# Optimization experiments

Measured on AMD Instinct MI355X. Metric: run time of the kernel, lower is better.

Reference implementation:

```python
import jax, jax.numpy as jnp
import numpy as np

N_MOTIF_PER_CLASS = 8
N_CLASS = 16
N_MOTIF = N_MOTIF_PER_CLASS * N_CLASS
TEMPERATURE = 0.2
TAU = 0.99
K2 = 32
EPS = 1e-4


def setup_inputs() -> dict:
    key = jax.random.key(0)
    k1, k2, k3 = jax.random.split(key, 3)
    N, H = 32768, 1024
    z = jax.random.normal(k1, (N, H), dtype=jnp.float32)
    Motif_Vector = jax.random.normal(k2, (N_MOTIF, H), dtype=jnp.float32)
    y = jax.random.randint(k3, (N,), 0, N_CLASS, dtype=jnp.int64)
    return {"z": z, "Motif_Vector": Motif_Vector, "y": y}


def euclidean_1(X, M):
    # squared euclidean distance via GEMM, then log-ratio similarity
    xp = X @ M.T                                     # [N, n_motif]
    distance = (-2.0 * xp
                + jnp.sum(X * X, axis=1, keepdims=True)
                + jnp.sum(M * M, axis=1)[None, :])
    similarity = jnp.log((distance + 1.0) / (distance + EPS))
    return similarity, distance


def reference(z, Motif_Vector, y):
    similarity, distance = euclidean_1(z, Motif_Vector)

    # mapping: motif j belongs to class j // n_motif_per_class
    motif_class = jnp.arange(N_MOTIF) // N_MOTIF_PER_CLASS   # [n_motif]
    true_motifs = (y[:, None] == motif_class[None, :])       # [N, n_motif]

    # contrastive loss (exact torch math: exp(sim/T), max over positives,
    # sum over negatives)
    sims = jnp.exp(similarity / TEMPERATURE)
    sim_pos = jnp.max(jnp.where(true_motifs, sims, -jnp.inf), axis=1)
    sim_neg_sum = jnp.sum(jnp.where(true_motifs, 0.0, sims), axis=1)
    loss = -jnp.mean(jnp.log(sim_pos / (sim_neg_sum + sim_pos)))

    # update_motif (update_type='topk', weighted_mean=False):
    # torch passes `distance` into filter_similar_graph and argsorts
    # descending, i.e. selects the K2 LARGEST distances among same-class
    # samples (faithful to source).
    masked = jnp.where(true_motifs.T, distance.T, -jnp.inf)  # [n_motif, N]
    _, idx = jax.lax.top_k(masked, K2)                       # [n_motif, K2]
    selected = z[idx]                                        # [n_motif, K2, H]
    new_motif = jnp.mean(selected, axis=1)                   # weights = 1/K2
    new_M = TAU * Motif_Vector + (1.0 - TAU) * new_motif

    return loss, new_M
```

## Files before the change

kernel.cpp:

```cpp
#include <hip/hip_runtime.h>
#include <cstdint>
#include <cmath>

#define NROWS 32768
#define HD    1024
#define NMOT  128
#define NCLS  16
#define KSEL  32
#define EPSV  1e-4f

typedef __attribute__((ext_vector_type(4))) float  f32x4;
typedef __attribute__((ext_vector_type(8))) __bf16 bf16x8;
typedef __attribute__((ext_vector_type(4))) __bf16 bf16x4;
typedef unsigned long long u64;

#define WS_MN   64
#define WS_MVBF 256
#define WS_CD   65792
#define WS_S1K  327936

static __device__ __forceinline__ float dot4(float4 v) {
    return v.x * v.x + v.y * v.y + v.z * v.z + v.w * v.w;
}

static __device__ __forceinline__ bf16x4 cvt4(float4 v) {
    bf16x4 t;
    t[0] = (__bf16)v.x; t[1] = (__bf16)v.y; t[2] = (__bf16)v.z; t[3] = (__bf16)v.w;
    return t;
}

static __device__ __forceinline__ u64 pack_key(float v, int idx) {
    unsigned int b = __float_as_uint(v);
    unsigned int mo = (b & 0x80000000u) ? ~b : (b | 0x80000000u);
    unsigned int khi = ~mo;
    return ((u64)khi << 32) | (unsigned int)idx;
}

__global__ __launch_bounds__(256) void prep_k(const float* __restrict__ mv,
                                              float* __restrict__ wsf,
                                              __bf16* __restrict__ mvbf) {
    const int j = blockIdx.x;
    const int k = threadIdx.x * 4;
    float4 v = *(const float4*)&mv[(size_t)j * HD + k];
    *(bf16x4*)&mvbf[(size_t)j * HD + k] = cvt4(v);
    float s = dot4(v);
#pragma unroll
    for (int o = 1; o < 64; o <<= 1) s += __shfl_xor(s, o, 64);
    __shared__ float red[4];
    if ((threadIdx.x & 63) == 0) red[threadIdx.x >> 6] = s;
    __syncthreads();
    if (threadIdx.x == 0) {
        wsf[WS_MN + j] = red[0] + red[1] + red[2] + red[3];
        if (j == 0) wsf[0] = 0.f;
    }
}

#define BM 64
#define BN 128
#define BK 32
#define NS (HD / BK)
#define SA 40

__global__ __launch_bounds__(256, 2) void gemm_fused(
    const float* __restrict__ z, const __bf16* __restrict__ mvbf,
    const float* __restrict__ mn, float* __restrict__ cd,
    const int* __restrict__ y, float* __restrict__ lossAcc) {
    __shared__ __bf16 As[2][BM * SA];
    __shared__ __bf16 Bs[2][BN * SA];
    __shared__ float  szn[BM];
    __shared__ int    ly[BM];
    __shared__ float  spm[2][BM];
    __shared__ float  sns[2][BM];

    const int tid  = threadIdx.x;
    const int row0 = blockIdx.x * BM;
    const int lane = tid & 63;
    const int wave = tid >> 6;
    const int wr   = wave >> 1;
    const int wc   = wave & 1;
    const int l15  = lane & 15;
    const int quad = lane >> 4;

    const int sq = tid & 7;
    const int sr = tid >> 3;
    const int bq = tid & 3;
    const int br = tid >> 2;

    if (tid < BM) ly[tid] = y[row0 + tid];

    f32x4 acc[2][4];
#pragma unroll
    for (int i = 0; i < 2; ++i)
#pragma unroll
        for (int j = 0; j < 4; ++j) acc[i][j] = (f32x4){0.f, 0.f, 0.f, 0.f};

    float zsq0 = 0.f, zsq1 = 0.f;

    const float*  zb = z + (size_t)(row0 + sr) * HD + sq * 4;
    const __bf16* bb = mvbf + (size_t)br * HD + bq * 8;

    float4 ra0[4], ra1[4];
    bf16x8 rb0[4], rb1[4];
#pragma unroll
    for (int s = 0; s < 4; ++s) {
        ra0[s] = *(const float4*)(zb + s * BK);
        ra1[s] = *(const float4*)(zb + s * BK + 32 * HD);
        rb0[s] = *(const bf16x8*)(bb + s * BK);
        rb1[s] = *(const bf16x8*)(bb + s * BK + 64 * HD);
    }
    *(bf16x4*)&As[0][sr * SA + sq * 4]        = cvt4(ra0[0]);
    *(bf16x4*)&As[0][(sr + 32) * SA + sq * 4] = cvt4(ra1[0]);
    *(bf16x8*)&Bs[0][br * SA + bq * 8]        = rb0[0];
    *(bf16x8*)&Bs[0][(br + 64) * SA + bq * 8] = rb1[0];
    zsq0 += dot4(ra0[0]); zsq1 += dot4(ra1[0]);
    ra0[0] = *(const float4*)(zb + 4 * BK);
    ra1[0] = *(const float4*)(zb + 4 * BK + 32 * HD);
    rb0[0] = *(const bf16x8*)(bb + 4 * BK);
    rb1[0] = *(const bf16x8*)(bb + 4 * BK + 64 * HD);
    __syncthreads();

    for (int it = 0; it < NS / 4; ++it) {
#pragma unroll
        for (int u = 0; u < 4; ++u) {
            const int kt = it * 4 + u;
            const int rbuf = kt & 1;
            const int ko = quad * 8;
            bf16x8 af[2], bfr[4];
#pragma unroll
            for (int i = 0; i < 2; ++i)
                af[i] = *(const bf16x8*)&As[rbuf][(wr * 32 + i * 16 + l15) * SA + ko];
#pragma unroll
            for (int j = 0; j < 4; ++j)
                bfr[j] = *(const bf16x8*)&Bs[rbuf][(wc * 64 + j * 16 + l15) * SA + ko];
            if (kt + 1 < NS) {
                const int w = (kt + 1) & 1;
                const int s = (kt + 1) & 3;
                *(bf16x4*)&As[w][sr * SA + sq * 4]        = cvt4(ra0[s]);
                *(bf16x4*)&As[w][(sr + 32) * SA + sq * 4] = cvt4(ra1[s]);
                *(bf16x8*)&Bs[w][br * SA + bq * 8]        = rb0[s];
                *(bf16x8*)&Bs[w][(br + 64) * SA + bq * 8] = rb1[s];
                zsq0 += dot4(ra0[s]); zsq1 += dot4(ra1[s]);
                if (kt + 5 < NS) {
                    const float*  zn = zb + (kt + 5) * BK;
                    const __bf16* bn = bb + (kt + 5) * BK;
                    ra0[s] = *(const float4*)(zn);
                    ra1[s] = *(const float4*)(zn + 32 * HD);
                    rb0[s] = *(const bf16x8*)(bn);
                    rb1[s] = *(const bf16x8*)(bn + 64 * HD);
                }
            }
#pragma unroll
            for (int i = 0; i < 2; ++i)
#pragma unroll
                for (int j = 0; j < 4; ++j)
                    acc[i][j] = __builtin_amdgcn_mfma_f32_16x16x32_bf16(
                        af[i], bfr[j], acc[i][j], 0, 0, 0);
            __syncthreads();
        }
    }

#pragma unroll
    for (int o = 1; o < 8; o <<= 1) {
        zsq0 += __shfl_xor(zsq0, o, 64);
        zsq1 += __shfl_xor(zsq1, o, 64);
    }
    if (sq == 0) { szn[sr] = zsq0; szn[sr + 32] = zsq1; }
    __syncthreads();

    f32x4 znv[2];
    int rcls[2][4];
#pragma unroll
    for (int i = 0; i < 2; ++i) {
        znv[i] = *(const f32x4*)&szn[wr * 32 + i * 16 + quad * 4];
#pragma unroll
        for (int reg = 0; reg < 4; ++reg)
            rcls[i][reg] = ly[wr * 32 + i * 16 + quad * 4 + reg];
    }
    float pm[2][4], ns[2][4];
#pragma unroll
    for (int i = 0; i < 2; ++i)
#pragma unroll
        for (int reg = 0; reg < 4; ++reg) { pm[i][reg] = 0.f; ns[i][reg] = 0.f; }

#pragma unroll
    for (int j = 0; j < 4; ++j) {
        const int c = wc * 64 + j * 16 + l15;
        const float mc = mn[c];
        const int ccls = c >> 3;
#pragma unroll
        for (int i = 0; i < 2; ++i) {
#pragma unroll
            for (int reg = 0; reg < 4; ++reg) {
                const int row = wr * 32 + i * 16 + quad * 4 + reg;
                float d = znv[i][reg] + mc - 2.f * acc[i][j][reg];
                float r = (d + 1.0f) * __builtin_amdgcn_rcpf(d + EPSV);
                float r2 = r * r;
                float s = r2 * r2 * r;
                if (ccls == rcls[i][reg]) {
                    pm[i][reg] = fmaxf(pm[i][reg], s);
                    cd[(size_t)(row0 + row) * 8 + (c & 7)] = d;
                } else {
                    ns[i][reg] += s;
                }
            }
        }
    }
#pragma unroll
    for (int o = 1; o < 16; o <<= 1) {
#pragma unroll
        for (int i = 0; i < 2; ++i)
#pragma unroll
            for (int reg = 0; reg < 4; ++reg) {
                pm[i][reg] = fmaxf(pm[i][reg], __shfl_xor(pm[i][reg], o, 64));
                ns[i][reg] += __shfl_xor(ns[i][reg], o, 64);
            }
    }
    if (l15 == 0) {
#pragma unroll
        for (int i = 0; i < 2; ++i)
#pragma unroll
            for (int reg = 0; reg < 4; ++reg) {
                const int row = wr * 32 + i * 16 + quad * 4 + reg;
                spm[wc][row] = pm[i][reg];
                sns[wc][row] = ns[i][reg];
            }
    }
    __syncthreads();
    if (tid < BM) {
        float p = fmaxf(spm[0][tid], spm[1][tid]);
        float nsum = sns[0][tid] + sns[1][tid];
        float li = logf((nsum + p) / p);
#pragma unroll
        for (int o = 1; o < 64; o <<= 1) li += __shfl_xor(li, o, 64);
        if (tid == 0) atomicAdd(lossAcc, li);
    }
}

__global__ __launch_bounds__(256) void sel1_k(const int* __restrict__ y,
                                              const float* __restrict__ cd,
                                              u64* __restrict__ s1k) {
    __shared__ u64 keys[512];
    __shared__ int cnt;

    const int bid = blockIdx.x;
    const int j = bid >> 3, chunk = bid & 7;
    const int cls = j >> 3, m8 = j & 7;
    const int tid = threadIdx.x;
    const int lane = tid & 63;
    if (tid == 0) cnt = 0;
    __syncthreads();

    const int base = chunk * 4096;
#pragma unroll
    for (int t = 0; t < 16; ++t) {
        const int i = base + t * 256 + tid;
        const bool pred = (y[i] == cls);
        const u64 m = __ballot(pred);
        int wbase = 0;
        if (lane == 0 && m) wbase = atomicAdd(&cnt, (int)__popcll(m));
        wbase = __shfl(wbase, 0, 64);
        if (pred) {
            const int p = wbase + (int)__popcll(m & ((1ull << lane) - 1ull));
            if (p < 512) keys[p] = pack_key(cd[(size_t)i * 8 + m8], i);
        }
    }
    __syncthreads();
    const int n = cnt < 512 ? cnt : 512;
    for (int t = tid; t < 512; t += 256)
        if (t >= n) keys[t] = ~0ull;
    __syncthreads();

    for (int k = 2; k <= 512; k <<= 1) {
        for (int jj = k >> 1; jj > 0; jj >>= 1) {
            const int i  = ((tid & ~(jj - 1)) << 1) | (tid & (jj - 1));
            const int ix = i | jj;
            const u64 A = keys[i], B = keys[ix];
            const bool up = ((i & k) == 0);
            if ((A > B) == up) { keys[i] = B; keys[ix] = A; }
            __syncthreads();
        }
    }
    if (tid < KSEL) s1k[(size_t)bid * KSEL + tid] = keys[tid];
}

__global__ __launch_bounds__(256) void merge_k(
    const float* __restrict__ z, const float* __restrict__ mv,
    const u64* __restrict__ s1k, const float* __restrict__ lossAcc,
    float* __restrict__ out) {
    __shared__ u64 keys[256];
    __shared__ int sel[KSEL];

    const int b = blockIdx.x;
    const int j = b >> 2, q = b & 3;
    const int tid = threadIdx.x;
    keys[tid] = s1k[(size_t)j * 256 + tid];
    __syncthreads();

    for (int k = 2; k <= 256; k <<= 1) {
        for (int jj = k >> 1; jj > 0; jj >>= 1) {
            if (tid < 128) {
                const int i  = ((tid & ~(jj - 1)) << 1) | (tid & (jj - 1));
                const int ix = i | jj;
                const u64 A = keys[i], B = keys[ix];
                const bool up = ((i & k) == 0);
                if ((A > B) == up) { keys[i] = B; keys[ix] = A; }
            }
            __syncthreads();
        }
    }
    if (tid < KSEL) sel[tid] = (int)(keys[tid] & 0xFFFFFFFFu);
    __syncthreads();

    const int h = q * 256 + tid;
    float s = 0.f;
#pragma unroll 8
    for (int r = 0; r < KSEL; ++r) s += z[(size_t)sel[r] * HD + h];
    out[1 + (size_t)j * HD + h] =
        0.99f * mv[(size_t)j * HD + h] + 0.01f * (s * (1.0f / KSEL));
    if (b == 0 && tid == 0) out[0] = lossAcc[0] * (1.0f / NROWS);
}

extern "C" void kernel_launch(void* const* d_in, const int* in_sizes, int n_in,
                              void* d_out, int out_size, void* d_ws, size_t ws_size,
                              hipStream_t stream) {
    const float* z  = (const float*)d_in[0];
    const float* mv = (const float*)d_in[1];
    const int*   y  = (const int*)d_in[2];
    float* out = (float*)d_out;
    float* wsf = (float*)d_ws;
    float*  mn   = wsf + WS_MN;
    __bf16* mvbf = (__bf16*)(wsf + WS_MVBF);
    float*  cd   = wsf + WS_CD;
    u64*    s1k  = (u64*)(wsf + WS_S1K);

    hipLaunchKernelGGL(prep_k,     dim3(NMOT),       dim3(256), 0, stream, mv, wsf, mvbf);
    hipLaunchKernelGGL(gemm_fused, dim3(NROWS / BM), dim3(256), 0, stream, z, mvbf, mn, cd, y, wsf);
    hipLaunchKernelGGL(sel1_k,     dim3(NMOT * 8),   dim3(256), 0, stream, y, cd, s1k);
    hipLaunchKernelGGL(merge_k,    dim3(NMOT * 4),   dim3(256), 0, stream, z, mv, s1k, wsf, out);
}
```

Measured before the change: 236.7 us.

## Precompute per-class row index lists and restructure two-stage top-k selection

Builds per-class, per-chunk lists of row indices once in the prep kernel, with 256 extra blocks scanning y. The first selection stage then gathers distances from the list instead of each of 128 motifs rescanning y, and sorts only 256 keys per block across 16 chunks. The merge stage sorts 512 candidates instead of 256. This cuts redundant scans of y and shrinks the first-stage sort, at the cost of a larger merge sort and an assumption that each chunk holds at most 256 same-class rows.

```diff
diff --git a/kernel.cpp b/kernel.cpp
--- a/kernel.cpp
+++ b/kernel.cpp
@@ -18,6 +18,9 @@
 #define WS_MVBF 256
 #define WS_CD   65792
 #define WS_S1K  327936
+#define WS_CL   459008
+#define WS_CCNT 524544
+#define CAPC    256
 
 static __device__ __forceinline__ float dot4(float4 v) {
     return v.x * v.x + v.y * v.y + v.z * v.z + v.w * v.w;
@@ -37,21 +40,50 @@
 }
 
 __global__ __launch_bounds__(256) void prep_k(const float* __restrict__ mv,
+                                              const int* __restrict__ y,
                                               float* __restrict__ wsf,
-                                              __bf16* __restrict__ mvbf) {
-    const int j = blockIdx.x;
-    const int k = threadIdx.x * 4;
-    float4 v = *(const float4*)&mv[(size_t)j * HD + k];
-    *(bf16x4*)&mvbf[(size_t)j * HD + k] = cvt4(v);
-    float s = dot4(v);
-#pragma unroll
-    for (int o = 1; o < 64; o <<= 1) s += __shfl_xor(s, o, 64);
-    __shared__ float red[4];
-    if ((threadIdx.x & 63) == 0) red[threadIdx.x >> 6] = s;
-    __syncthreads();
-    if (threadIdx.x == 0) {
-        wsf[WS_MN + j] = red[0] + red[1] + red[2] + red[3];
-        if (j == 0) wsf[0] = 0.f;
+                                              __bf16* __restrict__ mvbf,
+                                              int* __restrict__ clist,
+                                              int* __restrict__ ccnt) {
+    const int b = blockIdx.x;
+    const int tid = threadIdx.x;
+    if (b < NMOT) {
+        const int k = tid * 4;
+        float4 v = *(const float4*)&mv[(size_t)b * HD + k];
+        *(bf16x4*)&mvbf[(size_t)b * HD + k] = cvt4(v);
+        float s = dot4(v);
+#pragma unroll
+        for (int o = 1; o < 64; o <<= 1) s += __shfl_xor(s, o, 64);
+        __shared__ float red[4];
+        if ((tid & 63) == 0) red[tid >> 6] = s;
+        __syncthreads();
+        if (tid == 0) {
+            wsf[WS_MN + b] = red[0] + red[1] + red[2] + red[3];
+            if (b == 0) wsf[0] = 0.f;
+        }
+    } else {
+        __shared__ int cnt;
+        const int lid = b - NMOT;
+        const int cls = lid >> 4, chunk = lid & 15;
+        const int lane = tid & 63;
+        if (tid == 0) cnt = 0;
+        __syncthreads();
+        const int base = chunk * 2048;
+#pragma unroll
+        for (int t = 0; t < 8; ++t) {
+            const int i = base + t * 256 + tid;
+            const bool pred = (y[i] == cls);
+            const u64 m = __ballot(pred);
+            int wbase = 0;
+            if (lane == 0 && m) wbase = atomicAdd(&cnt, (int)__popcll(m));
+            wbase = __shfl(wbase, 0, 64);
+            if (pred) {
+                const int p = wbase + (int)__popcll(m & ((1ull << lane) - 1ull));
+                if (p < CAPC) clist[lid * CAPC + p] = i;
+            }
+        }
+        __syncthreads();
+        if (tid == 0) ccnt[lid] = cnt < CAPC ? cnt : CAPC;
     }
 }
 
@@ -236,38 +268,54 @@
     }
 }
 
-__global__ __launch_bounds__(256) void sel1_k(const int* __restrict__ y,
+__global__ __launch_bounds__(256) void sel1_k(const int* __restrict__ clist,
+                                              const int* __restrict__ ccnt,
                                               const float* __restrict__ cd,
                                               u64* __restrict__ s1k) {
+    __shared__ u64 keys[256];
+
+    const int bid = blockIdx.x;
+    const int j = bid >> 4, chunk = bid & 15;
+    const int cls = j >> 3, m8 = j & 7;
+    const int lid = cls * 16 + chunk;
+    const int tid = threadIdx.x;
+
+    const int n = ccnt[lid];
+    u64 key = ~0ull;
+    if (tid < n) {
+        const int idx = clist[lid * CAPC + tid];
+        key = pack_key(cd[(size_t)idx * 8 + m8], idx);
+    }
+    keys[tid] = key;
+    __syncthreads();
+
+    for (int k = 2; k <= 256; k <<= 1) {
+        for (int jj = k >> 1; jj > 0; jj >>= 1) {
+            if (tid < 128) {
+                const int i  = ((tid & ~(jj - 1)) << 1) | (tid & (jj - 1));
+                const int ix = i | jj;
+                const u64 A = keys[i], B = keys[ix];
+                const bool up = ((i & k) == 0);
+                if ((A > B) == up) { keys[i] = B; keys[ix] = A; }
+            }
+            __syncthreads();
+        }
+    }
+    if (tid < KSEL) s1k[(size_t)j * 512 + chunk * KSEL + tid] = keys[tid];
+}
+
+__global__ __launch_bounds__(256) void merge_k(
+    const float* __restrict__ z, const float* __restrict__ mv,
+    const u64* __restrict__ s1k, const float* __restrict__ lossAcc,
+    float* __restrict__ out) {
     __shared__ u64 keys[512];
-    __shared__ int cnt;
-
-    const int bid = blockIdx.x;
-    const int j = bid >> 3, chunk = bid & 7;
-    const int cls = j >> 3, m8 = j & 7;
+    __shared__ int sel[KSEL];
+
+    const int b = blockIdx.x;
+    const int j = b >> 2, q = b & 3;
     const int tid = threadIdx.x;
-    const int lane = tid & 63;
-    if (tid == 0) cnt = 0;
-    __syncthreads();
-
-    const int base = chunk * 4096;
-#pragma unroll
-    for (int t = 0; t < 16; ++t) {
-        const int i = base + t * 256 + tid;
-        const bool pred = (y[i] == cls);
-        const u64 m = __ballot(pred);
-        int wbase = 0;
-        if (lane == 0 && m) wbase = atomicAdd(&cnt, (int)__popcll(m));
-        wbase = __shfl(wbase, 0, 64);
-        if (pred) {
-            const int p = wbase + (int)__popcll(m & ((1ull << lane) - 1ull));
-            if (p < 512) keys[p] = pack_key(cd[(size_t)i * 8 + m8], i);
-        }
-    }
-    __syncthreads();
-    const int n = cnt < 512 ? cnt : 512;
-    for (int t = tid; t < 512; t += 256)
-        if (t >= n) keys[t] = ~0ull;
+    keys[tid]       = s1k[(size_t)j * 512 + tid];
+    keys[tid + 256] = s1k[(size_t)j * 512 + 256 + tid];
     __syncthreads();
 
     for (int k = 2; k <= 512; k <<= 1) {
@@ -280,34 +328,6 @@
             __syncthreads();
         }
     }
-    if (tid < KSEL) s1k[(size_t)bid * KSEL + tid] = keys[tid];
-}
-
-__global__ __launch_bounds__(256) void merge_k(
-    const float* __restrict__ z, const float* __restrict__ mv,
-    const u64* __restrict__ s1k, const float* __restrict__ lossAcc,
-    float* __restrict__ out) {
-    __shared__ u64 keys[256];
-    __shared__ int sel[KSEL];
-
-    const int b = blockIdx.x;
-    const int j = b >> 2, q = b & 3;
-    const int tid = threadIdx.x;
-    keys[tid] = s1k[(size_t)j * 256 + tid];
-    __syncthreads();
-
-    for (int k = 2; k <= 256; k <<= 1) {
-        for (int jj = k >> 1; jj > 0; jj >>= 1) {
-            if (tid < 128) {
-                const int i  = ((tid & ~(jj - 1)) << 1) | (tid & (jj - 1));
-                const int ix = i | jj;
-                const u64 A = keys[i], B = keys[ix];
-                const bool up = ((i & k) == 0);
-                if ((A > B) == up) { keys[i] = B; keys[ix] = A; }
-            }
-            __syncthreads();
-        }
-    }
     if (tid < KSEL) sel[tid] = (int)(keys[tid] & 0xFFFFFFFFu);
     __syncthreads();
 
@@ -328,13 +348,19 @@
     const int*   y  = (const int*)d_in[2];
     float* out = (float*)d_out;
     float* wsf = (float*)d_ws;
-    float*  mn   = wsf + WS_MN;
-    __bf16* mvbf = (__bf16*)(wsf + WS_MVBF);
-    float*  cd   = wsf + WS_CD;
-    u64*    s1k  = (u64*)(wsf + WS_S1K);
-
-    hipLaunchKernelGGL(prep_k,     dim3(NMOT),       dim3(256), 0, stream, mv, wsf, mvbf);
-    hipLaunchKernelGGL(gemm_fused, dim3(NROWS / BM), dim3(256), 0, stream, z, mvbf, mn, cd, y, wsf);
-    hipLaunchKernelGGL(sel1_k,     dim3(NMOT * 8),   dim3(256), 0, stream, y, cd, s1k);
-    hipLaunchKernelGGL(merge_k,    dim3(NMOT * 4),   dim3(256), 0, stream, z, mv, s1k, wsf, out);
-}
+    float*  mn    = wsf + WS_MN;
+    __bf16* mvbf  = (__bf16*)(wsf + WS_MVBF);
+    float*  cd    = wsf + WS_CD;
+    u64*    s1k   = (u64*)(wsf + WS_S1K);
+    int*    clist = (int*)(wsf + WS_CL);
+    int*    ccnt  = (int*)(wsf + WS_CCNT);
+
+    hipLaunchKernelGGL(prep_k,     dim3(NMOT + 256), dim3(256), 0, stream,
+                       mv, y, wsf, mvbf, clist, ccnt);
+    hipLaunchKernelGGL(gemm_fused, dim3(NROWS / BM), dim3(256), 0, stream,
+                       z, mvbf, mn, cd, y, wsf);
+    hipLaunchKernelGGL(sel1_k,     dim3(NMOT * 16),  dim3(256), 0, stream,
+                       clist, ccnt, cd, s1k);
+    hipLaunchKernelGGL(merge_k,    dim3(NMOT * 4),   dim3(256), 0, stream,
+                       z, mv, s1k, wsf, out);
+}
```

After: 231.4 us. 1.02x faster.
